# Kernel optimization log

Measured on AMD Instinct MI355X. Metric: run time of the kernel, lower is better.

Reference implementation:

```python
import jax, jax.numpy as jnp
import numpy as np

SCALE = 1.0
P0 = 0.1


def setup_inputs() -> dict:
    key = jax.random.key(0)
    k1, k2, k3, k4 = jax.random.split(key, 4)
    B, N, D, T, TM = 64, 2048, 128, 512, 512
    data = jax.random.normal(k1, (B, N, D), dtype=jnp.float32)
    targets = jax.random.normal(k2, (B, N), dtype=jnp.float32)
    W = jax.random.normal(k3, (D, T), dtype=jnp.float32)        # major task pool, (n_dims, n_tasks)
    W_minor = jax.random.normal(k4, (D, TM), dtype=jnp.float32)  # minor task pool
    return {"data": data, "targets": targets, "W": W, "W_minor": W_minor}


def reference(data, targets, W, W_minor):
    # data: (B, N, D); targets: (B, N); W: (D, T); W_minor: (D, TM)
    n_minor = W_minor.shape[1]
    W_all = jnp.concatenate([W, W_minor], axis=1)            # (D, T_total)
    XW = jnp.einsum('bnd,dt->bnt', data, W_all)              # (B, N, T_total)
    diff2 = (targets[..., None] - XW) ** 2                   # (B, N, T_total)
    # Prefix sum-of-squared-residuals: step i uses points 0..i-1 (step 0 -> zeros,
    # matching the original's zeros-prefix call).
    prefix = jnp.cumsum(diff2, axis=1)
    prefix = jnp.concatenate([jnp.zeros_like(prefix[:, :1]), prefix[:, :-1]], axis=1)
    # Log priors: original hardcodes log((1-p0)/3) for major tasks (kept faithfully).
    log_prior_major = float(np.log((1.0 - P0) / 3.0))
    log_prior_minor = float(np.log(P0 / n_minor))
    log_prior = jnp.concatenate([
        jnp.full((W.shape[1],), log_prior_major, dtype=data.dtype),
        jnp.full((n_minor,), log_prior_minor, dtype=data.dtype),
    ])                                                        # (T_total,)
    log_probs = -0.5 * prefix / (SCALE ** 2) + log_prior      # (B, N, T_total)
    weights = jax.nn.softmax(log_probs, axis=-1)              # posterior over tasks
    w_mmse = jnp.einsum('bnt,dt->bnd', weights, W_all)        # (B, N, D)
    preds = jnp.sum(data * w_mmse, axis=-1)                   # (B, N)
    return preds
```

## Files before the change

kernel.cpp:

```cpp
#include <hip/hip_runtime.h>

typedef _Float16 half8 __attribute__((ext_vector_type(8)));
typedef float floatx4 __attribute__((ext_vector_type(4)));

#define NB 64
#define NN 2048
#define ND 128
#define NT 1024
#define NC 16
#define NCHUNKS 128
#define NIV 64

#define ALPHA 0.84932184f
#define INV_ALPHA 1.17741002f
#define LP2_MAJOR (-1.7369655941662063f)
#define LP2_MINOR (-12.321928094887362f)

__device__ __forceinline__ float fexp2(float x) {
  float r;
  asm("v_exp_f32 %0, %1" : "=v"(r) : "v"(x));
  return r;
}

#define PIN8(x) asm volatile("" : "+v"(x))

template <int CTRL>
__device__ __forceinline__ float dppshr_add(float x) {
  int i = __builtin_bit_cast(int, x);
  int s = __builtin_amdgcn_update_dpp(0, i, CTRL, 0xF, 0xF, true);
  return x + __builtin_bit_cast(float, s);
}
__device__ __forceinline__ float scan16(float x) {
  x = dppshr_add<0x111>(x);
  x = dppshr_add<0x112>(x);
  x = dppshr_add<0x114>(x);
  x = dppshr_add<0x118>(x);
  return x;
}
__device__ __forceinline__ float bcast15(float x) {
  int i = __builtin_bit_cast(int, x);
  i = __builtin_amdgcn_ds_swizzle(i, 0x1F0);
  return __builtin_bit_cast(float, i);
}

__global__ void k_prep(const float* __restrict__ W, const float* __restrict__ Wm,
                       _Float16* __restrict__ Wph, _Float16* __restrict__ Wpl) {
  int idx = blockIdx.x * 256 + threadIdx.x;
  int t = idx >> 7, d = idx & 127;
  float x = (t < 512) ? W[d * 512 + t] : Wm[d * 512 + (t - 512)];
  x *= ALPHA;
  _Float16 h = (_Float16)x;
  _Float16 l = (_Float16)(x - (float)h);
  Wph[idx] = h;
  Wpl[idx] = l;
}

__global__ void k_prep_data(const float* __restrict__ data,
                            _Float16* __restrict__ Apk) {
  int idx = blockIdx.x * 256 + threadIdx.x;
  int l = idx & 63, kk = (idx >> 6) & 3, ch = (idx >> 8) & 127, b = idx >> 15;
  int row = ch * 16 + (l & 15);
  int dcol = kk * 32 + (l >> 4) * 8;
  const float* src = data + ((size_t)b * NN + row) * ND + dcol;
  floatx4 a0 = *(const floatx4*)src;
  floatx4 a1 = *(const floatx4*)(src + 4);
  half8 h, lo;
#pragma unroll
  for (int j = 0; j < 4; ++j) {
    h[j] = (_Float16)a0[j];
    lo[j] = (_Float16)(a0[j] - (float)h[j]);
    h[4 + j] = (_Float16)a1[j];
    lo[4 + j] = (_Float16)(a1[j] - (float)h[4 + j]);
  }
  size_t o = ((size_t)(b * 128 + ch)) * 4096 + kk * 512 + l * 8;
  *(half8*)(Apk + o) = h;
  *(half8*)(Apk + o + 2048) = lo;
}

__global__ __launch_bounds__(256, 2)
void k_fused(const _Float16* __restrict__ Apk, const float* __restrict__ targets,
             const _Float16* __restrict__ Wph, const _Float16* __restrict__ Wpl,
             floatx4* __restrict__ part) {
  int bid = blockIdx.x;
  int xcd = bid & 7, rest = bid >> 3;
  int tq = rest & 7, b = (rest >> 3) * 8 + xcd;
  int tid = threadIdx.x;
  int w = tid >> 6, l = tid & 63;
  int l15 = l & 15, lhi = l >> 4;
  int wavebase = tq * 128 + w * 32;

  half8 wh[2][4], wl[2][4];
#pragma unroll
  for (int tt = 0; tt < 2; ++tt)
#pragma unroll
    for (int kk = 0; kk < 4; ++kk) {
      int off = (wavebase + tt * 16 + l15) * 128 + kk * 32 + lhi * 8;
      wh[tt][kk] = *(const half8*)(Wph + off);
      wl[tt][kk] = *(const half8*)(Wpl + off);
    }
#pragma unroll
  for (int tt = 0; tt < 2; ++tt)
#pragma unroll
    for (int kk = 0; kk < 4; ++kk) { PIN8(wh[tt][kk]); PIN8(wl[tt][kk]); }

  float prior2 = (tq < 4) ? LP2_MAJOR : LP2_MINOR;
  floatx4 pmr0 = {prior2, prior2, prior2, prior2};
  floatx4 pmr1 = pmr0;

  const _Float16* abase = Apk + (size_t)b * 128 * 4096;
  const float* tgp = targets + (size_t)b * NN + l15;
  size_t pbase = (size_t)b * NN * 8 + tq;

  __shared__ _Float16 Abuf[2][8192];
  __shared__ floatx4 sm4[4][4][65];

  int t8 = tid * 8;

#define GEMM3(ACC, TT, AH, AL)                                                      \
  do {                                                                              \
    floatx4 hh = {0.f, 0.f, 0.f, 0.f};                                              \
    floatx4 hl = {0.f, 0.f, 0.f, 0.f};                                              \
    floatx4 lh = {0.f, 0.f, 0.f, 0.f};                                              \
    _Pragma("unroll")                                                               \
    for (int kk = 0; kk < 4; ++kk) {                                                \
      hh = __builtin_amdgcn_mfma_f32_16x16x32_f16(wh[TT][kk], AH[kk], hh, 0, 0, 0); \
      hl = __builtin_amdgcn_mfma_f32_16x16x32_f16(wh[TT][kk], AL[kk], hl, 0, 0, 0); \
      lh = __builtin_amdgcn_mfma_f32_16x16x32_f16(wl[TT][kk], AH[kk], lh, 0, 0, 0); \
    }                                                                               \
    ACC = (hh + hl) + lh;                                                           \
  } while (0)

#define EPI(A0, A1, SLOT, TGS)                                        \
  do {                                                                \
    floatx4 tg4 = {(TGS), (TGS), (TGS), (TGS)};                       \
    floatx4 d0 = tg4 - (A0), d1 = tg4 - (A1);                         \
    floatx4 q0 = d0 * d0, q1 = d1 * d1;                               \
    floatx4 i0, i1;                                                   \
    _Pragma("unroll")                                                 \
    for (int r = 0; r < 4; ++r) {                                     \
      i0[r] = scan16(q0[r]); i1[r] = scan16(q1[r]);                   \
    }                                                                 \
    floatx4 lp0 = pmr0 + (q0 - i0);                                   \
    floatx4 lp1 = pmr1 + (q1 - i1);                                   \
    _Pragma("unroll")                                                 \
    for (int r = 0; r < 4; ++r) {                                     \
      pmr0[r] -= bcast15(i0[r]); pmr1[r] -= bcast15(i1[r]);           \
    }                                                                 \
    float m = fmaxf(fmaxf(fmaxf(lp0[0], lp0[1]), fmaxf(lp0[2], lp0[3])), \
                    fmaxf(fmaxf(lp1[0], lp1[1]), fmaxf(lp1[2], lp1[3]))); \
    floatx4 m4 = {m, m, m, m};                                        \
    floatx4 x0 = lp0 - m4, x1 = lp1 - m4;                             \
    floatx4 e0, e1;                                                   \
    _Pragma("unroll")                                                 \
    for (int r = 0; r < 4; ++r) { e0[r] = fexp2(x0[r]); e1[r] = fexp2(x1[r]); } \
    floatx4 s1v = e0 + e1;                                            \
    floatx4 s2v = e0 * (A0) + e1 * (A1);                              \
    floatx4 outv;                                                     \
    outv[0] = m;                                                      \
    outv[1] = (s1v[0] + s1v[1]) + (s1v[2] + s1v[3]);                  \
    outv[2] = (s2v[0] + s2v[1]) + (s2v[2] + s2v[3]);                  \
    outv[3] = 0.f;                                                    \
    sm4[w][SLOT][l] = outv;                                           \
  } while (0)

#define MERGE(BASECH)                                                 \
  do {                                                                \
    if (tid < 64) {                                                   \
      int c4 = tid >> 4, row = tid & 15;                              \
      float M = -3.4e38f;                                             \
      _Pragma("unroll")                                               \
      for (int wv = 0; wv < 4; ++wv)                                  \
        _Pragma("unroll")                                             \
        for (int g = 0; g < 4; ++g)                                   \
          M = fmaxf(M, sm4[wv][c4][g * 16 + row][0]);                 \
      float S1 = 0.f, S2 = 0.f;                                       \
      _Pragma("unroll")                                               \
      for (int wv = 0; wv < 4; ++wv)                                  \
        _Pragma("unroll")                                             \
        for (int g = 0; g < 4; ++g) {                                 \
          floatx4 vv = sm4[wv][c4][g * 16 + row];                     \
          float e = fexp2(vv[0] - M);                                 \
          S1 = fmaf(vv[1], e, S1);                                    \
          S2 = fmaf(vv[2], e, S2);                                    \
        }                                                             \
      floatx4 v;                                                      \
      v[0] = M; v[1] = S1; v[2] = S2; v[3] = 0.f;                     \
      part[pbase + (size_t)(((BASECH) + c4) * 16 + row) * 8] = v;     \
    }                                                                 \
  } while (0)

#define LOADFRAGS(OFF)                                                \
  _Pragma("unroll")                                                   \
  for (int kk = 0; kk < 4; ++kk) {                                    \
    ah[kk] = *(const half8*)&Abuf[cur][(OFF) + kk * 512 + l * 8];     \
    al[kk] = *(const half8*)&Abuf[cur][(OFF) + 2048 + kk * 512 + l * 8]; \
  }

  half8 s0 = *(const half8*)(abase + t8);
  half8 s1_ = *(const half8*)(abase + 2048 + t8);
  half8 s2_ = *(const half8*)(abase + 4096 + t8);
  half8 s3 = *(const half8*)(abase + 6144 + t8);
  *(half8*)&Abuf[0][t8] = s0;
  *(half8*)&Abuf[0][2048 + t8] = s1_;
  *(half8*)&Abuf[0][4096 + t8] = s2_;
  *(half8*)&Abuf[0][6144 + t8] = s3;
  s0 = *(const half8*)(abase + 8192 + t8);
  s1_ = *(const half8*)(abase + 8192 + 2048 + t8);
  s2_ = *(const half8*)(abase + 8192 + 4096 + t8);
  s3 = *(const half8*)(abase + 8192 + 6144 + t8);
  __syncthreads();

  floatx4 pA0, pA1, pB0, pB1;
  float ptgA, ptgB;

  {
    int cur = 0;
    half8 ah[4], al[4];
    LOADFRAGS(0);
    GEMM3(pA0, 0, ah, al);
    GEMM3(pA1, 1, ah, al);
    LOADFRAGS(4096);
    GEMM3(pB0, 0, ah, al);
    GEMM3(pB1, 1, ah, al);
    ptgA = tgp[0] * ALPHA;
    ptgB = tgp[16] * ALPHA;
    *(half8*)&Abuf[1][t8] = s0;
    *(half8*)&Abuf[1][2048 + t8] = s1_;
    *(half8*)&Abuf[1][4096 + t8] = s2_;
    *(half8*)&Abuf[1][6144 + t8] = s3;
    const _Float16* pp = abase + 2 * 8192 + t8;
    s0 = *(const half8*)pp;
    s1_ = *(const half8*)(pp + 2048);
    s2_ = *(const half8*)(pp + 4096);
    s3 = *(const half8*)(pp + 6144);
    __syncthreads();
    tgp += 32;
  }

  for (int iv = 1; iv < NIV; ++iv) {
    int cur = iv & 1;
    half8 ah[4], al[4];
    floatx4 aA0, aA1, aB0, aB1;
    LOADFRAGS(0);
    GEMM3(aA0, 0, ah, al);
    GEMM3(aA1, 1, ah, al);
    LOADFRAGS(4096);
    GEMM3(aB0, 0, ah, al);
    GEMM3(aB1, 1, ah, al);
    float tgA = tgp[0] * ALPHA;
    float tgB = tgp[16] * ALPHA;

    *(half8*)&Abuf[cur ^ 1][t8] = s0;
    *(half8*)&Abuf[cur ^ 1][2048 + t8] = s1_;
    *(half8*)&Abuf[cur ^ 1][4096 + t8] = s2_;
    *(half8*)&Abuf[cur ^ 1][6144 + t8] = s3;
    {
      int pf = iv + 2 > 63 ? 63 : iv + 2;
      const _Float16* pp = abase + (size_t)pf * 8192 + t8;
      s0 = *(const half8*)pp;
      s1_ = *(const half8*)(pp + 2048);
      s2_ = *(const half8*)(pp + 4096);
      s3 = *(const half8*)(pp + 6144);
    }

    EPI(pA0, pA1, ((2 * iv - 2) & 3), ptgA);
    EPI(pB0, pB1, ((2 * iv - 1) & 3), ptgB);

    if (!(iv & 1)) {
      __syncthreads();
      MERGE(2 * iv - 4);
    }
    __syncthreads();

    pA0 = aA0; pA1 = aA1; pB0 = aB0; pB1 = aB1;
    ptgA = tgA; ptgB = tgB;
    tgp += 32;
  }

  EPI(pA0, pA1, 2, ptgA);
  EPI(pB0, pB1, 3, ptgB);
  __syncthreads();
  MERGE(124);

#undef EPI
#undef GEMM3
#undef MERGE
#undef LOADFRAGS
}

__global__ void k_combine(const floatx4* __restrict__ part, float* __restrict__ out) {
  int idx = blockIdx.x * 256 + threadIdx.x;
  const floatx4* p = part + (size_t)idx * 8;
  floatx4 v[8];
  float M = -3.4e38f;
#pragma unroll
  for (int j = 0; j < 8; ++j) { v[j] = p[j]; M = fmaxf(M, v[j][0]); }
  float s1 = 0.f, s2 = 0.f;
#pragma unroll
  for (int j = 0; j < 8; ++j) {
    float e = fexp2(v[j][0] - M);
    s1 += v[j][1] * e;
    s2 += v[j][2] * e;
  }
  out[idx] = s2 / s1 * INV_ALPHA;
}

extern "C" void kernel_launch(void* const* d_in, const int* in_sizes, int n_in,
                              void* d_out, int out_size, void* d_ws, size_t ws_size,
                              hipStream_t stream) {
  const float* data    = (const float*)d_in[0];
  const float* targets = (const float*)d_in[1];
  const float* W       = (const float*)d_in[2];
  const float* Wm      = (const float*)d_in[3];
  float* out = (float*)d_out;

  char* ws = (char*)d_ws;
  const size_t MB = 1u << 20;
  _Float16* Wph  = (_Float16*)ws;
  _Float16* Wpl  = (_Float16*)(ws + 256 * 1024);
  _Float16* Apk  = (_Float16*)(ws + 512 * 1024);
  floatx4* part  = (floatx4*)(ws + 512 * 1024 + 64 * MB);

  k_prep<<<512, 256, 0, stream>>>(W, Wm, Wph, Wpl);
  k_prep_data<<<8192, 256, 0, stream>>>(data, Apk);
  k_fused<<<NB * 8, 256, 0, stream>>>(Apk, targets, Wph, Wpl, part);
  k_combine<<<(NB * NN) / 256, 256, 0, stream>>>(part, out);
}
```

Baseline: 177.8 us.

## Split fused kernel work across 8 waves with one task tile each

The fused GEMM+softmax kernel now runs 512 threads per block, and each of 8 waves owns one 16-task tile instead of two. This halves the per-wave W registers, accumulators and epilogue work, raising occupancy through launch bounds (512,4). The per-wave row max and sums now need cross-lane shuffles, and the merge reads eight wave slots instead of sixteen groups. Staging loads are spread across more threads. The risk is extra shuffle cost and more threads contending at the barriers.

```diff
diff --git a/kernel.cpp b/kernel.cpp
--- a/kernel.cpp
+++ b/kernel.cpp
@@ -77,7 +77,7 @@
   *(half8*)(Apk + o + 2048) = lo;
 }
 
-__global__ __launch_bounds__(256, 2)
+__global__ __launch_bounds__(512, 4)
 void k_fused(const _Float16* __restrict__ Apk, const float* __restrict__ targets,
              const _Float16* __restrict__ Wph, const _Float16* __restrict__ Wpl,
              floatx4* __restrict__ part) {
@@ -87,80 +87,75 @@
   int tid = threadIdx.x;
   int w = tid >> 6, l = tid & 63;
   int l15 = l & 15, lhi = l >> 4;
-  int wavebase = tq * 128 + w * 32;
-
-  half8 wh[2][4], wl[2][4];
-#pragma unroll
-  for (int tt = 0; tt < 2; ++tt)
-#pragma unroll
-    for (int kk = 0; kk < 4; ++kk) {
-      int off = (wavebase + tt * 16 + l15) * 128 + kk * 32 + lhi * 8;
-      wh[tt][kk] = *(const half8*)(Wph + off);
-      wl[tt][kk] = *(const half8*)(Wpl + off);
-    }
-#pragma unroll
-  for (int tt = 0; tt < 2; ++tt)
-#pragma unroll
-    for (int kk = 0; kk < 4; ++kk) { PIN8(wh[tt][kk]); PIN8(wl[tt][kk]); }
+  int tbase = tq * 128 + w * 16;
+
+  half8 wh[4], wl[4];
+#pragma unroll
+  for (int kk = 0; kk < 4; ++kk) {
+    int off = (tbase + l15) * 128 + kk * 32 + lhi * 8;
+    wh[kk] = *(const half8*)(Wph + off);
+    wl[kk] = *(const half8*)(Wpl + off);
+  }
+#pragma unroll
+  for (int kk = 0; kk < 4; ++kk) { PIN8(wh[kk]); PIN8(wl[kk]); }
 
   float prior2 = (tq < 4) ? LP2_MAJOR : LP2_MINOR;
-  floatx4 pmr0 = {prior2, prior2, prior2, prior2};
-  floatx4 pmr1 = pmr0;
+  floatx4 pmr = {prior2, prior2, prior2, prior2};
 
   const _Float16* abase = Apk + (size_t)b * 128 * 4096;
   const float* tgp = targets + (size_t)b * NN + l15;
   size_t pbase = (size_t)b * NN * 8 + tq;
 
   __shared__ _Float16 Abuf[2][8192];
-  __shared__ floatx4 sm4[4][4][65];
+  __shared__ floatx4 sm4[8][4][17];
 
   int t8 = tid * 8;
 
-#define GEMM3(ACC, TT, AH, AL)                                                      \
-  do {                                                                              \
-    floatx4 hh = {0.f, 0.f, 0.f, 0.f};                                              \
-    floatx4 hl = {0.f, 0.f, 0.f, 0.f};                                              \
-    floatx4 lh = {0.f, 0.f, 0.f, 0.f};                                              \
-    _Pragma("unroll")                                                               \
-    for (int kk = 0; kk < 4; ++kk) {                                                \
-      hh = __builtin_amdgcn_mfma_f32_16x16x32_f16(wh[TT][kk], AH[kk], hh, 0, 0, 0); \
-      hl = __builtin_amdgcn_mfma_f32_16x16x32_f16(wh[TT][kk], AL[kk], hl, 0, 0, 0); \
-      lh = __builtin_amdgcn_mfma_f32_16x16x32_f16(wl[TT][kk], AH[kk], lh, 0, 0, 0); \
-    }                                                                               \
-    ACC = (hh + hl) + lh;                                                           \
+#define GEMM3(ACC, AH, AL)                                                     \
+  do {                                                                         \
+    floatx4 hh = {0.f, 0.f, 0.f, 0.f};                                         \
+    floatx4 hl = {0.f, 0.f, 0.f, 0.f};                                         \
+    floatx4 lh = {0.f, 0.f, 0.f, 0.f};                                         \
+    _Pragma("unroll")                                                          \
+    for (int kk = 0; kk < 4; ++kk) {                                           \
+      hh = __builtin_amdgcn_mfma_f32_16x16x32_f16(wh[kk], AH[kk], hh, 0, 0, 0);\
+      hl = __builtin_amdgcn_mfma_f32_16x16x32_f16(wh[kk], AL[kk], hl, 0, 0, 0);\
+      lh = __builtin_amdgcn_mfma_f32_16x16x32_f16(wl[kk], AH[kk], lh, 0, 0, 0);\
+    }                                                                          \
+    ACC = (hh + hl) + lh;                                                      \
   } while (0)
 
-#define EPI(A0, A1, SLOT, TGS)                                        \
+#define EPI(A, SLOT, TGS)                                             \
   do {                                                                \
     floatx4 tg4 = {(TGS), (TGS), (TGS), (TGS)};                       \
-    floatx4 d0 = tg4 - (A0), d1 = tg4 - (A1);                         \
-    floatx4 q0 = d0 * d0, q1 = d1 * d1;                               \
-    floatx4 i0, i1;                                                   \
+    floatx4 d = tg4 - (A);                                            \
+    floatx4 q = d * d;                                                \
+    floatx4 i0;                                                       \
     _Pragma("unroll")                                                 \
-    for (int r = 0; r < 4; ++r) {                                     \
-      i0[r] = scan16(q0[r]); i1[r] = scan16(q1[r]);                   \
+    for (int r = 0; r < 4; ++r) i0[r] = scan16(q[r]);                 \
+    floatx4 lp = pmr + (q - i0);                                      \
+    _Pragma("unroll")                                                 \
+    for (int r = 0; r < 4; ++r) pmr[r] -= bcast15(i0[r]);             \
+    float m = fmaxf(fmaxf(lp[0], lp[1]), fmaxf(lp[2], lp[3]));        \
+    m = fmaxf(m, __shfl_xor(m, 16));                                  \
+    m = fmaxf(m, __shfl_xor(m, 32));                                  \
+    floatx4 m4 = {m, m, m, m};                                        \
+    floatx4 x = lp - m4;                                              \
+    floatx4 e;                                                        \
+    _Pragma("unroll")                                                 \
+    for (int r = 0; r < 4; ++r) e[r] = fexp2(x[r]);                   \
+    float s1 = (e[0] + e[1]) + (e[2] + e[3]);                         \
+    float s2 = e[0] * (A)[0];                                         \
+    s2 = fmaf(e[1], (A)[1], s2);                                      \
+    s2 = fmaf(e[2], (A)[2], s2);                                      \
+    s2 = fmaf(e[3], (A)[3], s2);                                      \
+    s1 += __shfl_xor(s1, 16); s1 += __shfl_xor(s1, 32);               \
+    s2 += __shfl_xor(s2, 16); s2 += __shfl_xor(s2, 32);               \
+    if (l < 16) {                                                     \
+      floatx4 outv;                                                   \
+      outv[0] = m; outv[1] = s1; outv[2] = s2; outv[3] = 0.f;         \
+      sm4[w][SLOT][l] = outv;                                         \
     }                                                                 \
-    floatx4 lp0 = pmr0 + (q0 - i0);                                   \
-    floatx4 lp1 = pmr1 + (q1 - i1);                                   \
-    _Pragma("unroll")                                                 \
-    for (int r = 0; r < 4; ++r) {                                     \
-      pmr0[r] -= bcast15(i0[r]); pmr1[r] -= bcast15(i1[r]);           \
-    }                                                                 \
-    float m = fmaxf(fmaxf(fmaxf(lp0[0], lp0[1]), fmaxf(lp0[2], lp0[3])), \
-                    fmaxf(fmaxf(lp1[0], lp1[1]), fmaxf(lp1[2], lp1[3]))); \
-    floatx4 m4 = {m, m, m, m};                                        \
-    floatx4 x0 = lp0 - m4, x1 = lp1 - m4;                             \
-    floatx4 e0, e1;                                                   \
-    _Pragma("unroll")                                                 \
-    for (int r = 0; r < 4; ++r) { e0[r] = fexp2(x0[r]); e1[r] = fexp2(x1[r]); } \
-    floatx4 s1v = e0 + e1;                                            \
-    floatx4 s2v = e0 * (A0) + e1 * (A1);                              \
-    floatx4 outv;                                                     \
-    outv[0] = m;                                                      \
-    outv[1] = (s1v[0] + s1v[1]) + (s1v[2] + s1v[3]);                  \
-    outv[2] = (s2v[0] + s2v[1]) + (s2v[2] + s2v[3]);                  \
-    outv[3] = 0.f;                                                    \
-    sm4[w][SLOT][l] = outv;                                           \
   } while (0)
 
 #define MERGE(BASECH)                                                 \
@@ -169,20 +164,16 @@
       int c4 = tid >> 4, row = tid & 15;                              \
       float M = -3.4e38f;                                             \
       _Pragma("unroll")                                               \
-      for (int wv = 0; wv < 4; ++wv)                                  \
-        _Pragma("unroll")                                             \
-        for (int g = 0; g < 4; ++g)                                   \
-          M = fmaxf(M, sm4[wv][c4][g * 16 + row][0]);                 \
+      for (int wv = 0; wv < 8; ++wv)                                  \
+        M = fmaxf(M, sm4[wv][c4][row][0]);                            \
       float S1 = 0.f, S2 = 0.f;                                       \
       _Pragma("unroll")                                               \
-      for (int wv = 0; wv < 4; ++wv)                                  \
-        _Pragma("unroll")                                             \
-        for (int g = 0; g < 4; ++g) {                                 \
-          floatx4 vv = sm4[wv][c4][g * 16 + row];                     \
-          float e = fexp2(vv[0] - M);                                 \
-          S1 = fmaf(vv[1], e, S1);                                    \
-          S2 = fmaf(vv[2], e, S2);                                    \
-        }                                                             \
+      for (int wv = 0; wv < 8; ++wv) {                                \
+        floatx4 vv = sm4[wv][c4][row];                                \
+        float e = fexp2(vv[0] - M);                                   \
+        S1 = fmaf(vv[1], e, S1);                                      \
+        S2 = fmaf(vv[2], e, S2);                                      \
+      }                                                               \
       floatx4 v;                                                      \
       v[0] = M; v[1] = S1; v[2] = S2; v[3] = 0.f;                     \
       part[pbase + (size_t)(((BASECH) + c4) * 16 + row) * 8] = v;     \
@@ -197,42 +188,30 @@
   }
 
   half8 s0 = *(const half8*)(abase + t8);
-  half8 s1_ = *(const half8*)(abase + 2048 + t8);
-  half8 s2_ = *(const half8*)(abase + 4096 + t8);
-  half8 s3 = *(const half8*)(abase + 6144 + t8);
+  half8 s1_ = *(const half8*)(abase + 4096 + t8);
   *(half8*)&Abuf[0][t8] = s0;
-  *(half8*)&Abuf[0][2048 + t8] = s1_;
-  *(half8*)&Abuf[0][4096 + t8] = s2_;
-  *(half8*)&Abuf[0][6144 + t8] = s3;
-  s0 = *(const half8*)(abase + 8192 + t8);
-  s1_ = *(const half8*)(abase + 8192 + 2048 + t8);
-  s2_ = *(const half8*)(abase + 8192 + 4096 + t8);
-  s3 = *(const half8*)(abase + 8192 + 6144 + t8);
+  *(half8*)&Abuf[0][4096 + t8] = s1_;
+  s0 = *(const half8*)(abase + 2 * 4096 + t8);
+  s1_ = *(const half8*)(abase + 3 * 4096 + t8);
   __syncthreads();
 
-  floatx4 pA0, pA1, pB0, pB1;
+  floatx4 pA, pB;
   float ptgA, ptgB;
 
   {
     int cur = 0;
     half8 ah[4], al[4];
     LOADFRAGS(0);
-    GEMM3(pA0, 0, ah, al);
-    GEMM3(pA1, 1, ah, al);
+    GEMM3(pA, ah, al);
     LOADFRAGS(4096);
-    GEMM3(pB0, 0, ah, al);
-    GEMM3(pB1, 1, ah, al);
+    GEMM3(pB, ah, al);
     ptgA = tgp[0] * ALPHA;
     ptgB = tgp[16] * ALPHA;
     *(half8*)&Abuf[1][t8] = s0;
-    *(half8*)&Abuf[1][2048 + t8] = s1_;
-    *(half8*)&Abuf[1][4096 + t8] = s2_;
-    *(half8*)&Abuf[1][6144 + t8] = s3;
+    *(half8*)&Abuf[1][4096 + t8] = s1_;
     const _Float16* pp = abase + 2 * 8192 + t8;
     s0 = *(const half8*)pp;
-    s1_ = *(const half8*)(pp + 2048);
-    s2_ = *(const half8*)(pp + 4096);
-    s3 = *(const half8*)(pp + 6144);
+    s1_ = *(const half8*)(pp + 4096);
     __syncthreads();
     tgp += 32;
   }
@@ -240,31 +219,25 @@
   for (int iv = 1; iv < NIV; ++iv) {
     int cur = iv & 1;
     half8 ah[4], al[4];
-    floatx4 aA0, aA1, aB0, aB1;
+    floatx4 aA, aB;
     LOADFRAGS(0);
-    GEMM3(aA0, 0, ah, al);
-    GEMM3(aA1, 1, ah, al);
+    GEMM3(aA, ah, al);
     LOADFRAGS(4096);
-    GEMM3(aB0, 0, ah, al);
-    GEMM3(aB1, 1, ah, al);
+    GEMM3(aB, ah, al);
     float tgA = tgp[0] * ALPHA;
     float tgB = tgp[16] * ALPHA;
 
     *(half8*)&Abuf[cur ^ 1][t8] = s0;
-    *(half8*)&Abuf[cur ^ 1][2048 + t8] = s1_;
-    *(half8*)&Abuf[cur ^ 1][4096 + t8] = s2_;
-    *(half8*)&Abuf[cur ^ 1][6144 + t8] = s3;
+    *(half8*)&Abuf[cur ^ 1][4096 + t8] = s1_;
     {
       int pf = iv + 2 > 63 ? 63 : iv + 2;
       const _Float16* pp = abase + (size_t)pf * 8192 + t8;
       s0 = *(const half8*)pp;
-      s1_ = *(const half8*)(pp + 2048);
-      s2_ = *(const half8*)(pp + 4096);
-      s3 = *(const half8*)(pp + 6144);
+      s1_ = *(const half8*)(pp + 4096);
     }
 
-    EPI(pA0, pA1, ((2 * iv - 2) & 3), ptgA);
-    EPI(pB0, pB1, ((2 * iv - 1) & 3), ptgB);
+    EPI(pA, ((2 * iv - 2) & 3), ptgA);
+    EPI(pB, ((2 * iv - 1) & 3), ptgB);
 
     if (!(iv & 1)) {
       __syncthreads();
@@ -272,13 +245,13 @@
     }
     __syncthreads();
 
-    pA0 = aA0; pA1 = aA1; pB0 = aB0; pB1 = aB1;
+    pA = aA; pB = aB;
     ptgA = tgA; ptgB = tgB;
     tgp += 32;
   }
 
-  EPI(pA0, pA1, 2, ptgA);
-  EPI(pB0, pB1, 3, ptgB);
+  EPI(pA, 2, ptgA);
+  EPI(pB, 3, ptgB);
   __syncthreads();
   MERGE(124);
 
@@ -323,6 +296,6 @@
 
   k_prep<<<512, 256, 0, stream>>>(W, Wm, Wph, Wpl);
   k_prep_data<<<8192, 256, 0, stream>>>(data, Apk);
-  k_fused<<<NB * 8, 256, 0, stream>>>(Apk, targets, Wph, Wpl, part);
+  k_fused<<<NB * 8, 512, 0, stream>>>(Apk, targets, Wph, Wpl, part);
   k_combine<<<(NB * NN) / 256, 256, 0, stream>>>(part, out);
 }
```

New measurement: 188.1 us. 1.06x slower.
